# Kernel optimization log

Measured on AMD Instinct MI355X. Metric: run time of the kernel, lower is better.

## Reference

```python
import jax, jax.numpy as jnp
import numpy as np

P = 8  # patch_size hard-coded in the module


def conv1x1(x, W, b):
    # x: [B,C,H,W_], W: [O,C], b: [O]  (1x1 conv == per-pixel linear)
    return jnp.einsum('oc,bchw->bohw', W, x) + b[None, :, None, None]


def to_patch_tokens(t):
    # Replicates t.unfold(2,P,P).unfold(3,P,P).contiguous().view(B,-1,N)
    # t: [B,Cq,W,H] -> [B, Cq*P*P, N] with N = (W//P)*(H//P)
    B, Cq, Wd, Hd = t.shape
    Wp, Hp = Wd // P, Hd // P
    t = t.reshape(B, Cq, Wp, P, Hp, P).transpose(0, 1, 2, 4, 3, 5)  # [B,Cq,Wp,Hp,P,P]
    return t.reshape(B, Cq * P * P, Wp * Hp)


def setup_inputs() -> dict:
    key = jax.random.key(0)
    ks = jax.random.split(key, 10)
    B, C, Wd, Hd = 8, 64, 256, 256
    Cq = C // 8
    s_in = 1.0 / np.sqrt(C)
    s_out = 1.0 / np.sqrt(Cq)
    return {
        'x': jax.random.normal(ks[0], (B, C, Wd, Hd), jnp.float32),
        'Wq': jax.random.normal(ks[1], (Cq, C), jnp.float32) * s_in,
        'bq': jax.random.normal(ks[2], (Cq,), jnp.float32) * 0.01,
        'Wk': jax.random.normal(ks[3], (Cq, C), jnp.float32) * s_in,
        'bk': jax.random.normal(ks[4], (Cq,), jnp.float32) * 0.01,
        'Wv': jax.random.normal(ks[5], (Cq, C), jnp.float32) * s_in,
        'bv': jax.random.normal(ks[6], (Cq,), jnp.float32) * 0.01,
        'Wo': jax.random.normal(ks[7], (C, Cq), jnp.float32) * s_out,
        'bo': jax.random.normal(ks[8], (C,), jnp.float32) * 0.01,
        'gamma': jax.random.normal(ks[9], (1,), jnp.float32),
    }


def reference(x, Wq, bq, Wk, bk, Wv, bv, Wo, bo, gamma):
    B, C, Wd, Hd = x.shape
    Cq = C // 8
    q = to_patch_tokens(conv1x1(x, Wq, bq)).transpose(0, 2, 1)  # [B,N,M]
    k = to_patch_tokens(conv1x1(x, Wk, bk))                     # [B,M,N]
    v = to_patch_tokens(conv1x1(x, Wv, bv))                     # [B,M,N]
    N = k.shape[-1]  # d_k in source == number of patch tokens
    energy = jnp.einsum('bnm,bmk->bnk', q, k) / jnp.sqrt(jnp.float32(N))
    attn = jax.nn.softmax(energy, axis=-1)                      # [B,N,N]
    out = jnp.einsum('bmn,bjn->bmj', v, attn)                   # bmm(v, attn^T)
    out = out.transpose(0, 2, 1).reshape(B, Cq, Wd, Hd)
    out = conv1x1(out, Wo, bo)
    return gamma * out + x
```

## Files before the change

kernel.cpp:

```cpp
#include <hip/hip_runtime.h>
#include <stdint.h>

typedef unsigned short u16;
typedef unsigned int   u32;
typedef __attribute__((ext_vector_type(8))) short  short8;
typedef __attribute__((ext_vector_type(4))) float  floatx4;

__device__ __forceinline__ u16 f32_to_bf16(float f) {
  u32 u = __builtin_bit_cast(u32, f);
  u = (u + 0x7fffu + ((u >> 16) & 1u)) >> 16;
  return (u16)u;
}
__device__ __forceinline__ float bf16_to_f32(u16 h) {
  u32 u = ((u32)h) << 16;
  return __builtin_bit_cast(float, u);
}
__device__ __forceinline__ u32 pack2(float a, float b) {
  return (u32)f32_to_bf16(a) | ((u32)f32_to_bf16(b) << 16);
}

__device__ __forceinline__ void load_lds16(const u16* g, u16* l) {
  auto gp = (const __attribute__((address_space(1))) u32*)(uintptr_t)g;
  auto lp = (__attribute__((address_space(3))) u32*)(u32)(uintptr_t)l;
  __builtin_amdgcn_global_load_lds(gp, lp, 16, 0, 0);
}

__global__ __launch_bounds__(512) void qkv_kernel(
    const float* __restrict__ x,
    const float* __restrict__ Wq, const float* __restrict__ bq,
    const float* __restrict__ Wk, const float* __restrict__ bk,
    const float* __restrict__ Wv, const float* __restrict__ bv,
    u16* __restrict__ qt, u16* __restrict__ kt, u16* __restrict__ vm)
{
  __shared__ __align__(16) u16 qs[128 * 72];
  __shared__ __align__(16) u16 ks_[128 * 72];
  __shared__ __align__(16) u16 vs[64 * 128];

  const int wq = blockIdx.x;
  const int g  = blockIdx.y;
  const int b  = blockIdx.z;
  const int t  = threadIdx.x;
  const int wl = t >> 4;
  const int hg = t & 15;
  const int strip = hg >> 3, hq = hg & 7;
  const int w  = wq * 32 + wl;
  const int h0 = g * 16 + strip * 128 + hq * 2;

  float bqr[8], bkr[8], bvr[8];
#pragma unroll
  for (int i = 0; i < 8; i++) { bqr[i] = bq[i]; bkr[i] = bk[i]; bvr[i] = bv[i]; }

  float aq[2][8], ak[2][8], av[2][8];
#pragma unroll
  for (int j = 0; j < 2; j++)
#pragma unroll
    for (int i = 0; i < 8; i++) { aq[j][i] = 0.f; ak[j][i] = 0.f; av[j][i] = 0.f; }

  const float* xp = x + (size_t)b * 64 * 65536 + w * 256 + h0;
#pragma unroll 4
  for (int c = 0; c < 64; c++) {
    const float2 xv = *(const float2*)(xp + (size_t)c * 65536);
#pragma unroll
    for (int cq = 0; cq < 8; cq++) {
      const float wqv = Wq[cq * 64 + c];
      const float wkv = Wk[cq * 64 + c];
      const float wvv = Wv[cq * 64 + c];
      aq[0][cq] = fmaf(wqv, xv.x, aq[0][cq]);
      aq[1][cq] = fmaf(wqv, xv.y, aq[1][cq]);
      ak[0][cq] = fmaf(wkv, xv.x, ak[0][cq]);
      ak[1][cq] = fmaf(wkv, xv.y, ak[1][cq]);
      av[0][cq] = fmaf(wvv, xv.x, av[0][cq]);
      av[1][cq] = fmaf(wvv, xv.y, av[1][cq]);
    }
  }

  const int mc = ((wl >> 3) & 3) * 2 + strip;
#pragma unroll
  for (int j = 0; j < 2; j++) {
    const int h  = h0 + j;
    const int nl = ((h >> 3) & 1) * 64 + (w & 7) * 8 + (h & 7);
    uint4 qv, kv;
    qv.x = pack2(aq[j][0] + bqr[0], aq[j][1] + bqr[1]);
    qv.y = pack2(aq[j][2] + bqr[2], aq[j][3] + bqr[3]);
    qv.z = pack2(aq[j][4] + bqr[4], aq[j][5] + bqr[5]);
    qv.w = pack2(aq[j][6] + bqr[6], aq[j][7] + bqr[7]);
    kv.x = pack2(ak[j][0] + bkr[0], ak[j][1] + bkr[1]);
    kv.y = pack2(ak[j][2] + bkr[2], ak[j][3] + bkr[3]);
    kv.z = pack2(ak[j][4] + bkr[4], ak[j][5] + bkr[5]);
    kv.w = pack2(ak[j][6] + bkr[6], ak[j][7] + bkr[7]);
    *(uint4*)(qs  + nl * 72 + mc * 8) = qv;
    *(uint4*)(ks_ + nl * 72 + mc * 8) = kv;
#pragma unroll
    for (int cq = 0; cq < 8; cq++)
      vs[(cq * 8 + mc) * 128 + nl] = f32_to_bf16(av[j][cq] + bvr[cq]);
  }
  __syncthreads();

#pragma unroll
  for (int i = 0; i < 2; i++) {
    const int idx = i * 512 + t;
    const int nl2 = idx >> 3, cq2 = idx & 7;
    const size_t row = (size_t)b * 1024 + g * 128 + nl2;
    const u16* qr = qs  + nl2 * 72 + cq2;
    const u16* kr = ks_ + nl2 * 72 + cq2;
    uint4 qv, kv;
    qv.x = (u32)qr[0]  | ((u32)qr[8]  << 16);
    qv.y = (u32)qr[16] | ((u32)qr[24] << 16);
    qv.z = (u32)qr[32] | ((u32)qr[40] << 16);
    qv.w = (u32)qr[48] | ((u32)qr[56] << 16);
    kv.x = (u32)kr[0]  | ((u32)kr[8]  << 16);
    kv.y = (u32)kr[16] | ((u32)kr[24] << 16);
    kv.z = (u32)kr[32] | ((u32)kr[40] << 16);
    kv.w = (u32)kr[48] | ((u32)kr[56] << 16);
    *(uint4*)(qt + row * 512 + wq * 64 + cq2 * 8) = qv;
    *(uint4*)(kt + row * 512 + wq * 64 + cq2 * 8) = kv;
    const int pr = idx >> 4, l16 = idx & 15;
    const int mrow = (pr >> 3) * 64 + wq * 8 + (pr & 7);
    *(uint4*)(vm + ((size_t)b * 512 + mrow) * 1024 + g * 128 + l16 * 8) =
        *(const uint4*)(vs + pr * 128 + l16 * 8);
  }
}

template <int FMW>
__global__ __launch_bounds__(512) void gemm_nt(
    const u16* __restrict__ A, const u16* __restrict__ Bm, u16* __restrict__ Cm,
    int M, int N, int K, float scale)
{
  constexpr int BM = FMW * 32;
  constexpr int NA = BM / 64;
  __shared__ __align__(16) u16 As[2][BM * 64];
  __shared__ __align__(16) u16 Bs[2][128 * 64];

  const int bz = blockIdx.x, bn = blockIdx.y, bm = blockIdx.z;
  const int t = threadIdx.x;
  const int lane = t & 63, wid = t >> 6;
  const int wm = wid & 1, wn = wid >> 1;
  const int m0 = bm * BM, n0 = bn * 128;

  const u16* Ab = A + (size_t)bz * M * K + (size_t)m0 * K;
  const u16* Bb = Bm + (size_t)bz * N * K + (size_t)n0 * K;

  floatx4 acc[FMW][2];
#pragma unroll
  for (int i = 0; i < FMW; i++)
#pragma unroll
    for (int j = 0; j < 2; j++) acc[i][j] = (floatx4){0.f, 0.f, 0.f, 0.f};

  const int srow = wid * 8 + (lane >> 3);
  const int scol = (((lane & 7) ^ ((lane >> 3) & 7)) << 3);
  const int l15 = lane & 15, quad = lane >> 4;
  const int cxor = (l15 & 7) << 3;

#pragma unroll
  for (int i = 0; i < NA; i++)
    load_lds16(Ab + (size_t)(i * 64 + srow) * K + scol, As[0] + (i * 64 + wid * 8) * 64);
#pragma unroll
  for (int i = 0; i < 2; i++)
    load_lds16(Bb + (size_t)(i * 64 + srow) * K + scol, Bs[0] + (i * 64 + wid * 8) * 64);
  __syncthreads();

  const int nk = K >> 6;
#pragma unroll 2
  for (int kk = 0; kk < nk; kk++) {
    const int cur = kk & 1;
    if (kk + 1 < nk) {
      const int k1 = (kk + 1) << 6;
#pragma unroll
      for (int i = 0; i < NA; i++)
        load_lds16(Ab + (size_t)(i * 64 + srow) * K + k1 + scol,
                   As[cur ^ 1] + (i * 64 + wid * 8) * 64);
#pragma unroll
      for (int i = 0; i < 2; i++)
        load_lds16(Bb + (size_t)(i * 64 + srow) * K + k1 + scol,
                   Bs[cur ^ 1] + (i * 64 + wid * 8) * 64);
    }
#pragma unroll
    for (int ks = 0; ks < 2; ks++) {
      const int koff = (ks * 32 + quad * 8) ^ cxor;
      short8 a[FMW], b[2];
#pragma unroll
      for (int f = 0; f < FMW; f++)
        a[f] = *(const short8*)(As[cur] + (wm * FMW * 16 + f * 16 + l15) * 64 + koff);
#pragma unroll
      for (int f = 0; f < 2; f++)
        b[f] = *(const short8*)(Bs[cur] + (wn * 32 + f * 16 + l15) * 64 + koff);
#pragma unroll
      for (int fm = 0; fm < FMW; fm++)
#pragma unroll
        for (int fn = 0; fn < 2; fn++)
          acc[fm][fn] = __builtin_amdgcn_mfma_f32_16x16x32_bf16(a[fm], b[fn], acc[fm][fn], 0, 0, 0);
    }
    __syncthreads();
  }

  u16* Cb = Cm + (size_t)bz * M * N;
#pragma unroll
  for (int fm = 0; fm < FMW; fm++)
#pragma unroll
    for (int fn = 0; fn < 2; fn++)
#pragma unroll
      for (int r = 0; r < 4; r++) {
        int row = m0 + wm * FMW * 16 + fm * 16 + quad * 4 + r;
        int col = n0 + wn * 32 + fn * 16 + l15;
        Cb[(size_t)row * N + col] = f32_to_bf16(scale * acc[fm][fn][r]);
      }
}

__global__ __launch_bounds__(256) void softmax_kernel(u16* __restrict__ EP)
{
  const int r = (blockIdx.x << 2) + (threadIdx.x >> 6);
  const int lane = threadIdx.x & 63;
  u16* row = EP + (size_t)r * 1024;
  const uint4* rp = (const uint4*)row;

  uint4 v0 = rp[lane * 2];
  uint4 v1 = rp[lane * 2 + 1];
  const u32 wds[8] = {v0.x, v0.y, v0.z, v0.w, v1.x, v1.y, v1.z, v1.w};
  float e[16];
#pragma unroll
  for (int i = 0; i < 8; i++) {
    e[2 * i]     = bf16_to_f32((u16)wds[i]);
    e[2 * i + 1] = bf16_to_f32((u16)(wds[i] >> 16));
  }

  float mx = e[0];
#pragma unroll
  for (int i = 1; i < 16; i++) mx = fmaxf(mx, e[i]);
#pragma unroll
  for (int off = 32; off > 0; off >>= 1) mx = fmaxf(mx, __shfl_xor(mx, off));

  float s = 0.f;
#pragma unroll
  for (int i = 0; i < 16; i++) { e[i] = __expf(e[i] - mx); s += e[i]; }
#pragma unroll
  for (int off = 32; off > 0; off >>= 1) s += __shfl_xor(s, off);

  const float inv = 1.0f / s;
  uint4 o0, o1;
  o0.x = pack2(e[0] * inv,  e[1] * inv);
  o0.y = pack2(e[2] * inv,  e[3] * inv);
  o0.z = pack2(e[4] * inv,  e[5] * inv);
  o0.w = pack2(e[6] * inv,  e[7] * inv);
  o1.x = pack2(e[8] * inv,  e[9] * inv);
  o1.y = pack2(e[10] * inv, e[11] * inv);
  o1.z = pack2(e[12] * inv, e[13] * inv);
  o1.w = pack2(e[14] * inv, e[15] * inv);
  ((uint4*)row)[lane * 2]     = o0;
  ((uint4*)row)[lane * 2 + 1] = o1;
}

__global__ __launch_bounds__(256) void out_kernel(
    const float* __restrict__ x, const u16* __restrict__ OT,
    const float* __restrict__ Wo, const float* __restrict__ bo,
    const float* __restrict__ gammap, float* __restrict__ out)
{
  const int gb = blockIdx.x;
  const int osel = gb & 1;
  const int q2 = (gb >> 1) * 256 + threadIdx.x;
  const int b = q2 >> 15;
  const int rem = (q2 & 32767) * 2;
  const float gmv = gammap[0];

  const u16* otb = OT + (size_t)b * 524288;
  const int m0 = rem & 511;
  const int nbase = rem >> 9;
  float oc[8][2];
#pragma unroll
  for (int cq = 0; cq < 8; cq++) {
    ushort2 hv = *(const ushort2*)(otb + (size_t)(cq * 128 + nbase) * 512 + m0);
    oc[cq][0] = bf16_to_f32(hv.x);
    oc[cq][1] = bf16_to_f32(hv.y);
  }

  const size_t obase = (size_t)b * 4194304 + rem + (size_t)osel * 32 * 65536;
  const float* xb = x + obase;
  float* ob = out + obase;
  const int o0 = osel * 32;
#pragma unroll 4
  for (int oo = 0; oo < 32; oo++) {
    const int o = o0 + oo;
    const float2 xv = *(const float2*)(xb + (size_t)oo * 65536);
    const float bv = bo[o];
    float a0 = bv, a1 = bv;
#pragma unroll
    for (int cq = 0; cq < 8; cq++) {
      const float wv = Wo[o * 8 + cq];
      a0 = fmaf(wv, oc[cq][0], a0);
      a1 = fmaf(wv, oc[cq][1], a1);
    }
    float2 rv;
    rv.x = fmaf(gmv, a0, xv.x);
    rv.y = fmaf(gmv, a1, xv.y);
    *(float2*)(ob + (size_t)oo * 65536) = rv;
  }
}

extern "C" void kernel_launch(void* const* d_in, const int* in_sizes, int n_in,
                              void* d_out, int out_size, void* d_ws, size_t ws_size,
                              hipStream_t stream) {
  const float* x  = (const float*)d_in[0];
  const float* Wq = (const float*)d_in[1];
  const float* bq = (const float*)d_in[2];
  const float* Wk = (const float*)d_in[3];
  const float* bk = (const float*)d_in[4];
  const float* Wv = (const float*)d_in[5];
  const float* bv = (const float*)d_in[6];
  const float* Wo = (const float*)d_in[7];
  const float* bo = (const float*)d_in[8];
  const float* gm = (const float*)d_in[9];
  float* out = (float*)d_out;

  u16* qt = (u16*)d_ws;
  u16* kt = qt + 4194304;
  u16* vm = kt + 4194304;
  u16* EP = vm + 4194304;
  u16* OT = qt;

  qkv_kernel<<<dim3(8, 8, 8), 512, 0, stream>>>(x, Wq, bq, Wk, bk, Wv, bv, qt, kt, vm);
  gemm_nt<4><<<dim3(8, 8, 8), 512, 0, stream>>>(qt, kt, EP, 1024, 1024, 512, 0.03125f);
  softmax_kernel<<<2048, 256, 0, stream>>>(EP);
  gemm_nt<2><<<dim3(8, 4, 16), 512, 0, stream>>>(EP, vm, OT, 1024, 512, 1024, 1.0f);
  out_kernel<<<2048, 256, 0, stream>>>(x, OT, Wo, bo, gm, out);
}
```

Before: 323.9 us.

## Remap QKV projection blocks to contiguous rows with swizzled LDS staging

The QKV projection kernel now gives each block 8 full-width row segments of 128 pixels, so each 64-thread wavefront reads a contiguous 512-byte run of x per channel instead of short strided pieces. Per-channel results are staged in shared memory using an XOR swizzle to limit bank conflicts, then gathered into the patch-token layouts for q, k and v. The v output is written as contiguous 32-bit stores covering whole token ranges. The launch grid changes to match the new mapping, and this carries a risk of index-mapping errors in the patch permutation.

```diff
diff --git a/kernel.cpp b/kernel.cpp
--- a/kernel.cpp
+++ b/kernel.cpp
@@ -24,6 +24,8 @@
   auto lp = (__attribute__((address_space(3))) u32*)(u32)(uintptr_t)l;
   __builtin_amdgcn_global_load_lds(gp, lp, 16, 0, 0);
 }
+
+__device__ __forceinline__ int swz(int tk) { return tk ^ ((tk >> 3) & 56); }
 
 __global__ __launch_bounds__(512) void qkv_kernel(
     const float* __restrict__ x,
@@ -32,19 +34,18 @@
     const float* __restrict__ Wv, const float* __restrict__ bv,
     u16* __restrict__ qt, u16* __restrict__ kt, u16* __restrict__ vm)
 {
-  __shared__ __align__(16) u16 qs[128 * 72];
-  __shared__ __align__(16) u16 ks_[128 * 72];
-  __shared__ __align__(16) u16 vs[64 * 128];
-
-  const int wq = blockIdx.x;
-  const int g  = blockIdx.y;
+  __shared__ __align__(16) u16 qs[8 * 1024];
+  __shared__ __align__(16) u16 ks_[8 * 1024];
+  __shared__ __align__(16) u16 vs[8 * 1024];
+
+  const int wg = blockIdx.x;
+  const int s  = blockIdx.y;
   const int b  = blockIdx.z;
   const int t  = threadIdx.x;
-  const int wl = t >> 4;
-  const int hg = t & 15;
-  const int strip = hg >> 3, hq = hg & 7;
-  const int w  = wq * 32 + wl;
-  const int h0 = g * 16 + strip * 128 + hq * 2;
+  const int wrow = t >> 6;
+  const int hl2  = (t & 63) * 2;
+  const int w  = wg * 8 + wrow;
+  const int h  = s * 128 + hl2;
 
   float bqr[8], bkr[8], bvr[8];
 #pragma unroll
@@ -56,7 +57,7 @@
 #pragma unroll
     for (int i = 0; i < 8; i++) { aq[j][i] = 0.f; ak[j][i] = 0.f; av[j][i] = 0.f; }
 
-  const float* xp = x + (size_t)b * 64 * 65536 + w * 256 + h0;
+  const float* xp = x + (size_t)b * 64 * 65536 + w * 256 + h;
 #pragma unroll 4
   for (int c = 0; c < 64; c++) {
     const float2 xv = *(const float2*)(xp + (size_t)c * 65536);
@@ -74,50 +75,42 @@
     }
   }
 
-  const int mc = ((wl >> 3) & 3) * 2 + strip;
-#pragma unroll
-  for (int j = 0; j < 2; j++) {
-    const int h  = h0 + j;
-    const int nl = ((h >> 3) & 1) * 64 + (w & 7) * 8 + (h & 7);
+  const int tk0 = ((hl2 >> 3) << 6) | (wrow << 3) | (hl2 & 7);
+  const int st  = swz(tk0);
+#pragma unroll
+  for (int cq = 0; cq < 8; cq++) {
+    *(u32*)(qs  + cq * 1024 + st) = pack2(aq[0][cq] + bqr[cq], aq[1][cq] + bqr[cq]);
+    *(u32*)(ks_ + cq * 1024 + st) = pack2(ak[0][cq] + bkr[cq], ak[1][cq] + bkr[cq]);
+    *(u32*)(vs  + cq * 1024 + st) = pack2(av[0][cq] + bvr[cq], av[1][cq] + bvr[cq]);
+  }
+  __syncthreads();
+
+  const int wq = wg >> 2;
+  const int mc = (wg & 3) * 2 + s;
+  const int colbase = wq * 64 + mc * 8;
+
+#pragma unroll
+  for (int i = 0; i < 2; i++) {
+    const int tk = i * 512 + t;
+    const int sk = swz(tk);
     uint4 qv, kv;
-    qv.x = pack2(aq[j][0] + bqr[0], aq[j][1] + bqr[1]);
-    qv.y = pack2(aq[j][2] + bqr[2], aq[j][3] + bqr[3]);
-    qv.z = pack2(aq[j][4] + bqr[4], aq[j][5] + bqr[5]);
-    qv.w = pack2(aq[j][6] + bqr[6], aq[j][7] + bqr[7]);
-    kv.x = pack2(ak[j][0] + bkr[0], ak[j][1] + bkr[1]);
-    kv.y = pack2(ak[j][2] + bkr[2], ak[j][3] + bkr[3]);
-    kv.z = pack2(ak[j][4] + bkr[4], ak[j][5] + bkr[5]);
-    kv.w = pack2(ak[j][6] + bkr[6], ak[j][7] + bkr[7]);
-    *(uint4*)(qs  + nl * 72 + mc * 8) = qv;
-    *(uint4*)(ks_ + nl * 72 + mc * 8) = kv;
-#pragma unroll
-    for (int cq = 0; cq < 8; cq++)
-      vs[(cq * 8 + mc) * 128 + nl] = f32_to_bf16(av[j][cq] + bvr[cq]);
-  }
-  __syncthreads();
-
-#pragma unroll
-  for (int i = 0; i < 2; i++) {
-    const int idx = i * 512 + t;
-    const int nl2 = idx >> 3, cq2 = idx & 7;
-    const size_t row = (size_t)b * 1024 + g * 128 + nl2;
-    const u16* qr = qs  + nl2 * 72 + cq2;
-    const u16* kr = ks_ + nl2 * 72 + cq2;
-    uint4 qv, kv;
-    qv.x = (u32)qr[0]  | ((u32)qr[8]  << 16);
-    qv.y = (u32)qr[16] | ((u32)qr[24] << 16);
-    qv.z = (u32)qr[32] | ((u32)qr[40] << 16);
-    qv.w = (u32)qr[48] | ((u32)qr[56] << 16);
-    kv.x = (u32)kr[0]  | ((u32)kr[8]  << 16);
-    kv.y = (u32)kr[16] | ((u32)kr[24] << 16);
-    kv.z = (u32)kr[32] | ((u32)kr[40] << 16);
-    kv.w = (u32)kr[48] | ((u32)kr[56] << 16);
-    *(uint4*)(qt + row * 512 + wq * 64 + cq2 * 8) = qv;
-    *(uint4*)(kt + row * 512 + wq * 64 + cq2 * 8) = kv;
-    const int pr = idx >> 4, l16 = idx & 15;
-    const int mrow = (pr >> 3) * 64 + wq * 8 + (pr & 7);
-    *(uint4*)(vm + ((size_t)b * 512 + mrow) * 1024 + g * 128 + l16 * 8) =
-        *(const uint4*)(vs + pr * 128 + l16 * 8);
+    qv.x = (u32)qs[sk]        | ((u32)qs[1024 + sk] << 16);
+    qv.y = (u32)qs[2048 + sk] | ((u32)qs[3072 + sk] << 16);
+    qv.z = (u32)qs[4096 + sk] | ((u32)qs[5120 + sk] << 16);
+    qv.w = (u32)qs[6144 + sk] | ((u32)qs[7168 + sk] << 16);
+    kv.x = (u32)ks_[sk]        | ((u32)ks_[1024 + sk] << 16);
+    kv.y = (u32)ks_[2048 + sk] | ((u32)ks_[3072 + sk] << 16);
+    kv.z = (u32)ks_[4096 + sk] | ((u32)ks_[5120 + sk] << 16);
+    kv.w = (u32)ks_[6144 + sk] | ((u32)ks_[7168 + sk] << 16);
+    *(uint4*)(qt + ((size_t)b * 1024 + tk) * 512 + colbase) = qv;
+    *(uint4*)(kt + ((size_t)b * 1024 + tk) * 512 + colbase) = kv;
+  }
+
+#pragma unroll
+  for (int cq = 0; cq < 8; cq++) {
+    const int mrow = cq * 64 + wq * 8 + mc;
+    const u32 val = *(const u32*)(vs + cq * 1024 + swz(2 * t));
+    *(u32*)(vm + ((size_t)b * 512 + mrow) * 1024 + 2 * t) = val;
   }
 }
 
@@ -316,7 +309,7 @@
   u16* EP = vm + 4194304;
   u16* OT = qt;
 
-  qkv_kernel<<<dim3(8, 8, 8), 512, 0, stream>>>(x, Wq, bq, Wk, bk, Wv, bv, qt, kt, vm);
+  qkv_kernel<<<dim3(32, 2, 8), 512, 0, stream>>>(x, Wq, bq, Wk, bk, Wv, bv, qt, kt, vm);
   gemm_nt<4><<<dim3(8, 8, 8), 512, 0, stream>>>(qt, kt, EP, 1024, 1024, 512, 0.03125f);
   softmax_kernel<<<2048, 256, 0, stream>>>(EP);
   gemm_nt<2><<<dim3(8, 4, 16), 512, 0, stream>>>(EP, vm, OT, 1024, 512, 1024, 1.0f);
```

New measurement: 323.4 us. No clear change (-0.2%).
